# Performance work log

Hardware: AMD Instinct MI355X
Metric: run time of the kernel (lower is better)

## Reference

```python
import jax, jax.numpy as jnp
import numpy as np

B, T, C, H = 1, 4096, 3072, 24
D = C // H  # 128


def _make_rope_freqs(t, d):
    # comfy-style rotation matrices: [t, d//2, 2, 2] with rows [[cos,-sin],[sin,cos]]
    half = d // 2
    inv = 1.0 / (10000.0 ** (np.arange(half, dtype=np.float64) / half))
    ang = np.arange(t, dtype=np.float64)[:, None] * inv[None, :]
    cos, sin = np.cos(ang), np.sin(ang)
    f = np.stack([np.stack([cos, -sin], -1), np.stack([sin, cos], -1)], -2)
    return jnp.asarray(f, jnp.float32)


def setup_inputs() -> dict:
    key = jax.random.key(0)
    ks = jax.random.split(key, 6)
    s = 0.02  # typical init scale
    x = jax.random.normal(ks[0], (B, T, C), jnp.float32)
    context = jax.random.normal(ks[1], (B, T, C), jnp.float32)
    Wq = jax.random.normal(ks[2], (C, C), jnp.float32) * s
    Wk = jax.random.normal(ks[3], (C, C), jnp.float32) * s
    Wv = jax.random.normal(ks[4], (C, C), jnp.float32) * s
    Wo = jax.random.normal(ks[5], (C, C), jnp.float32) * s
    freqs = _make_rope_freqs(T, D)  # [T, D//2, 2, 2]
    return {"x": x, "context": context, "freqs": freqs,
            "Wq": Wq, "Wk": Wk, "Wv": Wv, "Wo": Wo}


def _apply_rope(t, freqs):
    # t: [B, T, H, D]; freqs: [T, D//2, 2, 2]
    b, tt, h, d = t.shape
    tr = t.reshape(b, tt, h, d // 2, 1, 2)
    f = freqs[:, None]  # [T, 1, D//2, 2, 2] -> broadcast over B, H
    out = f[..., 0] * tr[..., 0] + f[..., 1] * tr[..., 1]  # [B,T,H,D//2,2]
    return out.reshape(b, tt, h, d)


def reference(x, context, freqs, Wq, Wk, Wv, Wo):
    # QKV projections (torch Linear: y = x @ W.T), kept in BTHD layout
    q = (x @ Wq.T).reshape(B, T, H, D)
    k = (context @ Wk.T).reshape(B, -1, H, D)
    v = (context @ Wv.T).reshape(B, -1, H, D)
    # RoPE on q and k
    q = _apply_rope(q, freqs)
    k = _apply_rope(k, freqs)
    # SDPA, non-causal, scale 1/sqrt(D) (jax expects BTNH layout)
    out = jax.nn.dot_product_attention(q, k, v)
    return out.reshape(B, T, C) @ Wo.T
```

## Files before the change

### kernel.cpp

```cpp
#include <hip/hip_runtime.h>
#include <hip/hip_bf16.h>

#define TT 4096
#define CC 3072
#define HH 24
#define DD 128

typedef __bf16 bf16;
typedef __attribute__((ext_vector_type(8))) __bf16 bf16x8;
typedef __attribute__((ext_vector_type(4))) __bf16 bf16x4;
typedef __attribute__((ext_vector_type(4))) float f32x4;
typedef __attribute__((ext_vector_type(16))) float f32x16;
typedef __attribute__((ext_vector_type(4))) unsigned uint32x4;

#define MFMA(a,b,c)   __builtin_amdgcn_mfma_f32_16x16x32_bf16((a),(b),(c),0,0,0)
#define MFMA32(a,b,c) __builtin_amdgcn_mfma_f32_32x32x16_bf16((a),(b),(c),0,0,0)

static __device__ __forceinline__ unsigned cvtpk(float lo, float hi) {
  unsigned r;
  asm("v_cvt_pk_bf16_f32 %0, %1, %2" : "=v"(r) : "v"(lo), "v"(hi));
  return r;
}
static __device__ __forceinline__ float max3f(float a, float b, float c) {
  float r;
  asm("v_max3_f32 %0, %1, %2, %3" : "=v"(r) : "v"(a), "v"(b), "v"(c));
  return r;
}
static __device__ __forceinline__ void plswap(unsigned &x, unsigned &y) {
  asm volatile("v_permlane32_swap_b32 %0, %1" : "+v"(x), "+v"(y));
}

template<int ABF, int OBF>
__global__ __launch_bounds__(256, 2)
void gemm_nt(const void* __restrict__ Ap, const float* __restrict__ Bp,
             void* __restrict__ Cp, int M, int N, int K) {
  __shared__ bf16 As[2][128][40];
  __shared__ bf16 Bs[2][128][40];
  const int tid = threadIdx.x;
  const int lane = tid & 63, wid = tid >> 6;
  const int m0 = blockIdx.y * 128, n0 = blockIdx.x * 128;
  const int wr = (wid >> 1) * 64, wc = (wid & 1) * 64;
  const int r = lane & 15, g = lane >> 4;
  const float* Af = (const float*)Ap;
  const bf16*  Ab = (const bf16*)Ap;

  f32x4 acc[4][4] = {};
  f32x4 pa[4], pb[4];
  bf16x8 qa[2];

  const int NT = K >> 5;

  auto load_tiles = [&](int kt) {
    const int kk = kt * 32;
    if constexpr (ABF) {
      #pragma unroll
      for (int j = 0; j < 2; ++j) {
        int c = tid + 256*j, row = c >> 2, kc = c & 3;
        qa[j] = *(const bf16x8*)(Ab + (size_t)(m0+row)*K + kk + kc*8);
      }
    } else {
      #pragma unroll
      for (int j = 0; j < 4; ++j) {
        int c = tid + 256*j, row = c >> 3, kc = c & 7;
        pa[j] = *(const f32x4*)(Af + (size_t)(m0+row)*K + kk + kc*4);
      }
    }
    #pragma unroll
    for (int j = 0; j < 4; ++j) {
      int c = tid + 256*j, row = c >> 3, kc = c & 7;
      pb[j] = *(const f32x4*)(Bp + (size_t)(n0+row)*K + kk + kc*4);
    }
  };

  auto write_tiles = [&](int buf) {
    if constexpr (ABF) {
      #pragma unroll
      for (int j = 0; j < 2; ++j) {
        int c = tid + 256*j, row = c >> 2, kc = c & 3;
        *(bf16x8*)&As[buf][row][kc*8] = qa[j];
      }
    } else {
      #pragma unroll
      for (int j = 0; j < 4; ++j) {
        int c = tid + 256*j, row = c >> 3, kc = c & 7;
        bf16x4 b;
        b[0]=(bf16)pa[j][0]; b[1]=(bf16)pa[j][1]; b[2]=(bf16)pa[j][2]; b[3]=(bf16)pa[j][3];
        *(bf16x4*)&As[buf][row][kc*4] = b;
      }
    }
    #pragma unroll
    for (int j = 0; j < 4; ++j) {
      int c = tid + 256*j, row = c >> 3, kc = c & 7;
      bf16x4 b;
      b[0]=(bf16)pb[j][0]; b[1]=(bf16)pb[j][1]; b[2]=(bf16)pb[j][2]; b[3]=(bf16)pb[j][3];
      *(bf16x4*)&Bs[buf][row][kc*4] = b;
    }
  };

  load_tiles(0);
  write_tiles(0);
  __syncthreads();

  for (int kt = 0; kt < NT; ++kt) {
    const int cur = kt & 1;
    if (kt + 1 < NT) load_tiles(kt + 1);
    bf16x8 af[4], bfr[4];
    #pragma unroll
    for (int m = 0; m < 4; ++m) af[m]  = *(const bf16x8*)&As[cur][wr + m*16 + r][g*8];
    #pragma unroll
    for (int n = 0; n < 4; ++n) bfr[n] = *(const bf16x8*)&Bs[cur][wc + n*16 + r][g*8];
    #pragma unroll
    for (int m = 0; m < 4; ++m)
      #pragma unroll
      for (int n = 0; n < 4; ++n)
        acc[m][n] = MFMA(af[m], bfr[n], acc[m][n]);
    if (kt + 1 < NT) write_tiles((kt + 1) & 1);
    __syncthreads();
  }

  #pragma unroll
  for (int m = 0; m < 4; ++m)
    #pragma unroll
    for (int n = 0; n < 4; ++n) {
      const int col = n0 + wc + n*16 + r;
      #pragma unroll
      for (int j = 0; j < 4; ++j) {
        const int row = m0 + wr + m*16 + g*4 + j;
        float v = acc[m][n][j];
        if constexpr (OBF) ((bf16*)Cp)[(size_t)row*N + col] = (bf16)v;
        else               ((float*)Cp)[(size_t)row*N + col] = v;
      }
    }
}

__global__ __launch_bounds__(256)
void rope_kernel(bf16* __restrict__ X, const float* __restrict__ F, float scale) {
  const int i = blockIdx.x * 256 + threadIdx.x;
  const size_t e8 = (size_t)i * 8;
  const int t  = (int)(e8 / CC);
  const int c  = (int)(e8 % CC);
  const int hc = c & (DD - 1);
  const float4* f = (const float4*)(F + (size_t)t*256 + (hc>>1)*4);
  bf16x8 v = *(const bf16x8*)(X + e8);
  bf16x8 o;
  #pragma unroll
  for (int p = 0; p < 4; ++p) {
    float x0 = (float)v[2*p], x1 = (float)v[2*p+1];
    float4 ff = f[p];
    o[2*p]   = (bf16)((ff.x*x0 + ff.y*x1) * scale);
    o[2*p+1] = (bf16)((ff.z*x0 + ff.w*x1) * scale);
  }
  *(bf16x8*)(X + e8) = o;
}

__global__ __launch_bounds__(256)
void transpose_v(const bf16* __restrict__ V, bf16* __restrict__ Vt) {
  __shared__ bf16 tile[64 * 128];
  const int t0 = blockIdx.x * 64, h = blockIdx.y;
  const int tid = threadIdx.x;
  #pragma unroll
  for (int j = 0; j < 4; ++j) {
    int c = tid + 256*j, t = c >> 4, c16 = c & 15;
    uint4 val = *(const uint4*)(V + (size_t)(t0+t)*CC + h*DD + c16*8);
    int sw = ((t & 7) ^ ((t >> 3) & 7)) << 4;
    *(uint4*)((char*)tile + t*256 + ((c16*16) ^ sw)) = val;
  }
  __syncthreads();
  #pragma unroll
  for (int j = 0; j < 4; ++j) {
    int c = tid + 256*j, d = c >> 3, c8 = c & 7;
    bf16x8 o;
    #pragma unroll
    for (int i = 0; i < 8; ++i) {
      int t = c8*8 + i;
      int sw = ((t & 7) ^ ((t >> 3) & 7)) << 4;
      o[i] = *(const bf16*)((char*)tile + t*256 + ((d*2) ^ sw));
    }
    *(bf16x8*)(Vt + (size_t)(h*DD + d)*TT + t0 + c8*8) = o;
  }
}

__global__ __launch_bounds__(256, 3)
void attn_kernel(const bf16* __restrict__ Q, const bf16* __restrict__ Kb,
                 const bf16* __restrict__ Vt, bf16* __restrict__ O) {
  __shared__ bf16 Ks[64 * 128];
  __shared__ bf16 Vs[128 * 64];

  const int tid = threadIdx.x, lane = tid & 63, wid = tid >> 6;
  const int c31 = lane & 31, g2 = lane >> 5;

  const int bid = blockIdx.x;
  const int fid = (bid & 7) * 96 + (bid >> 3);
  const int h = fid >> 5, qt = fid & 31;
  const int qrow = qt * 128 + wid * 32 + c31;

  bf16x8 aq[8];
  {
    const bf16* qp = Q + (size_t)qrow * CC + h * DD + g2 * 8;
    #pragma unroll
    for (int d0 = 0; d0 < 8; ++d0) aq[d0] = *(const bf16x8*)(qp + d0 * 16);
  }

  float m_ = -1e30f, l_ = 0.f;
  f32x16 o_[4] = {};

  auto stage = [&](int kv0) {
    uint4 kr[4], vr4[4];
    #pragma unroll
    for (int j = 0; j < 4; ++j) {
      int cc = tid + 256*j, row = cc >> 4, c16 = cc & 15;
      kr[j] = *(const uint4*)(Kb + (size_t)(kv0 + row) * CC + h * DD + c16 * 8);
    }
    #pragma unroll
    for (int j = 0; j < 4; ++j) {
      int cc = tid + 256*j, row = cc >> 3, c8 = cc & 7;
      vr4[j] = *(const uint4*)(Vt + (size_t)(h * DD + row) * TT + kv0 + c8 * 8);
    }
    #pragma unroll
    for (int j = 0; j < 4; ++j) {
      int cc = tid + 256*j, row = cc >> 4, c16 = cc & 15;
      *(uint4*)((char*)Ks + row * 256 + ((c16 * 16) ^ ((row & 15) << 4))) = kr[j];
    }
    #pragma unroll
    for (int j = 0; j < 4; ++j) {
      int cc = tid + 256*j, row = cc >> 3, c8 = cc & 7;
      *(uint4*)((char*)Vs + row * 128 + ((c8 * 16) ^ ((row & 7) << 4))) = vr4[j];
    }
  };

  const int NT = TT / 64;
  for (int t = 0; t < NT; ++t) {
    if (t) __syncthreads();
    stage(t * 64);
    __syncthreads();

    f32x16 s[2] = {};
    __builtin_amdgcn_s_setprio(1);
    #pragma unroll
    for (int d0 = 0; d0 < 8; ++d0) {
      #pragma unroll
      for (int tt = 0; tt < 2; ++tt) {
        const int kvr = tt * 32 + c31;
        bf16x8 ak = *(const bf16x8*)((const char*)Ks + kvr * 256 +
                                     ((d0 * 32 + g2 * 16) ^ ((kvr & 15) << 4)));
        s[tt] = MFMA32(ak, aq[d0], s[tt]);
      }
    }
    __builtin_amdgcn_s_setprio(0);

    float mx = fmaxf(s[0][0], s[0][1]);
    #pragma unroll
    for (int i = 2; i < 16; i += 2) mx = max3f(mx, s[0][i], s[0][i+1]);
    #pragma unroll
    for (int i = 0; i < 16; i += 2) mx = max3f(mx, s[1][i], s[1][i+1]);
    mx = fmaxf(mx, __shfl_xor(mx, 32, 64));
    if (!__all(mx <= m_ + 8.f)) {
      float mn = fmaxf(m_, mx);
      float al = __builtin_amdgcn_exp2f(m_ - mn);
      l_ *= al;
      #pragma unroll
      for (int d0 = 0; d0 < 4; ++d0) o_[d0] *= al;
      m_ = mn;
    }

    unsigned w0[8], w1[8];
    float rs = 0.f;
    #pragma unroll
    for (int jj = 0; jj < 8; ++jj) {
      float a0 = __builtin_amdgcn_exp2f(s[0][2*jj] - m_);
      float b0 = __builtin_amdgcn_exp2f(s[0][2*jj+1] - m_);
      float a1 = __builtin_amdgcn_exp2f(s[1][2*jj] - m_);
      float b1 = __builtin_amdgcn_exp2f(s[1][2*jj+1] - m_);
      rs += (a0 + b0) + (a1 + b1);
      w0[jj] = cvtpk(a0, b0);
      w1[jj] = cvtpk(a1, b1);
    }
    rs += __shfl_xor(rs, 32, 64);
    l_ += rs;

    bf16x8 pb[4];
    #pragma unroll
    for (int t2 = 0; t2 < 4; ++t2) {
      const int jA = (t2 & 1) * 4;
      unsigned x0, y0, x1, y1;
      if (t2 < 2) { x0 = w0[jA]; y0 = w0[jA+2]; x1 = w0[jA+1]; y1 = w0[jA+3]; }
      else        { x0 = w1[jA]; y0 = w1[jA+2]; x1 = w1[jA+1]; y1 = w1[jA+3]; }
      plswap(x0, y0);
      plswap(x1, y1);
      uint32x4 uu; uu[0] = x0; uu[1] = x1; uu[2] = y0; uu[3] = y1;
      pb[t2] = __builtin_bit_cast(bf16x8, uu);
    }

    __builtin_amdgcn_s_setprio(1);
    #pragma unroll
    for (int d0 = 0; d0 < 4; ++d0) {
      const int vr = d0 * 32 + c31;
      #pragma unroll
      for (int t2 = 0; t2 < 4; ++t2) {
        bf16x8 av = *(const bf16x8*)((const char*)Vs + vr * 128 +
                                     ((t2 * 32 + g2 * 16) ^ ((vr & 7) << 4)));
        o_[d0] = MFMA32(av, pb[t2], o_[d0]);
      }
    }
    __builtin_amdgcn_s_setprio(0);
  }

  const float inv = 1.f / l_;
  bf16* orow = O + (size_t)qrow * CC + h * DD;
  #pragma unroll
  for (int d0 = 0; d0 < 4; ++d0)
    #pragma unroll
    for (int q4 = 0; q4 < 4; ++q4) {
      uint2 val;
      val.x = cvtpk(o_[d0][q4*4 + 0] * inv, o_[d0][q4*4 + 1] * inv);
      val.y = cvtpk(o_[d0][q4*4 + 2] * inv, o_[d0][q4*4 + 3] * inv);
      *(uint2*)(orow + d0*32 + q4*8 + g2*4) = val;
    }
}

extern "C" void kernel_launch(void* const* d_in, const int* in_sizes, int n_in,
                              void* d_out, int out_size, void* d_ws, size_t ws_size,
                              hipStream_t stream) {
  const float* x   = (const float*)d_in[0];
  const float* ctx = (const float*)d_in[1];
  const float* fr  = (const float*)d_in[2];
  const float* Wq  = (const float*)d_in[3];
  const float* Wk  = (const float*)d_in[4];
  const float* Wv  = (const float*)d_in[5];
  const float* Wo  = (const float*)d_in[6];
  float* out = (float*)d_out;
  char* ws = (char*)d_ws;

  const size_t SZ = (size_t)TT * CC * sizeof(bf16);
  bf16* Qb  = (bf16*)(ws);
  bf16* Kbf = (bf16*)(ws + SZ);
  bf16* Vb  = (bf16*)(ws + 2*SZ);
  bf16* Vtb = (bf16*)(ws + 3*SZ);
  bf16* Ob  = Vb;

  dim3 gg(CC/128, TT/128);
  gemm_nt<0,1><<<gg, 256, 0, stream>>>(x,   Wq, Qb,  TT, CC, CC);
  gemm_nt<0,1><<<gg, 256, 0, stream>>>(ctx, Wk, Kbf, TT, CC, CC);
  gemm_nt<0,1><<<gg, 256, 0, stream>>>(ctx, Wv, Vb,  TT, CC, CC);

  const int rblocks = (TT*CC/8)/256;
  rope_kernel<<<rblocks, 256, 0, stream>>>(Qb,  fr, 0.12751743314942355f);
  rope_kernel<<<rblocks, 256, 0, stream>>>(Kbf, fr, 1.0f);

  transpose_v<<<dim3(TT/64, HH), 256, 0, stream>>>(Vb, Vtb);
  attn_kernel<<<dim3(768), 256, 0, stream>>>(Qb, Kbf, Vtb, Ob);

  gemm_nt<1,0><<<gg, 256, 0, stream>>>(Ob, Wo, out, TT, CC, CC);
}
```

Baseline: 827.3 us.

## Pre-convert inputs to bf16, use direct-to-LDS GEMM loads, prefetch attention KV

Adds a bf16 conversion pass for x, context and all four weight matrices, then runs a new GEMM that streams bf16 tiles straight into LDS with global_load_lds instead of loading fp32 through registers and converting in-loop. The attention kernel now issues the next KV tile's global loads before computing on the current one, overlapping memory latency with MFMA work. The bf16 path is used only when the workspace is large enough and falls back to the old path otherwise. The new GEMM is single-buffered with two barriers per k-step, and the conversion kernels add extra memory traffic.

```diff
diff --git a/kernel.cpp b/kernel.cpp
--- a/kernel.cpp
+++ b/kernel.cpp
@@ -28,6 +28,78 @@
 }
 static __device__ __forceinline__ void plswap(unsigned &x, unsigned &y) {
   asm volatile("v_permlane32_swap_b32 %0, %1" : "+v"(x), "+v"(y));
+}
+static __device__ __forceinline__ void gl16(const bf16* g, bf16* l) {
+  __builtin_amdgcn_global_load_lds(
+      (const __attribute__((address_space(1))) unsigned int*)(g),
+      (__attribute__((address_space(3))) unsigned int*)(l), 16, 0, 0);
+}
+
+__global__ __launch_bounds__(256)
+void cvt_bf16(const float* __restrict__ in, bf16* __restrict__ out, int n8) {
+  int i = blockIdx.x * 256 + threadIdx.x;
+  const int stride = gridDim.x * 256;
+  for (; i < n8; i += stride) {
+    const float4* p = (const float4*)(in + (size_t)i * 8);
+    float4 a = p[0], b = p[1];
+    bf16x8 o;
+    o[0]=(bf16)a.x; o[1]=(bf16)a.y; o[2]=(bf16)a.z; o[3]=(bf16)a.w;
+    o[4]=(bf16)b.x; o[5]=(bf16)b.y; o[6]=(bf16)b.z; o[7]=(bf16)b.w;
+    *(bf16x8*)(out + (size_t)i * 8) = o;
+  }
+}
+
+template<int OBF>
+__global__ __launch_bounds__(256, 2)
+void gemm_bt(const bf16* __restrict__ A, const bf16* __restrict__ B,
+             void* __restrict__ Cp, int M, int N, int K) {
+  __shared__ bf16 As[128 * 32];
+  __shared__ bf16 Bs[128 * 32];
+  const int tid = threadIdx.x, lane = tid & 63, wid = tid >> 6;
+  const int m0 = blockIdx.y * 128, n0 = blockIdx.x * 128;
+  const int wr = (wid >> 1) * 64, wc = (wid & 1) * 64;
+  const int r = lane & 15, g = lane >> 4;
+  const int srow = lane >> 2, scol = (lane & 3) * 8;
+
+  f32x4 acc[4][4] = {};
+  const int NT = K >> 5;
+
+  for (int kt = 0; kt < NT; ++kt) {
+    const int kk = kt << 5;
+    if (kt) __syncthreads();
+    #pragma unroll
+    for (int j = 0; j < 2; ++j) {
+      const int base = (wid * 2 + j) * 16;
+      gl16(A + (size_t)(m0 + base + srow) * K + kk + scol, As + base * 32);
+      gl16(B + (size_t)(n0 + base + srow) * K + kk + scol, Bs + base * 32);
+    }
+    __syncthreads();
+
+    bf16x8 af[4], bfr[4];
+    #pragma unroll
+    for (int m = 0; m < 4; ++m) af[m]  = *(const bf16x8*)&As[(wr + m*16 + r)*32 + g*8];
+    #pragma unroll
+    for (int n = 0; n < 4; ++n) bfr[n] = *(const bf16x8*)&Bs[(wc + n*16 + r)*32 + g*8];
+    #pragma unroll
+    for (int m = 0; m < 4; ++m)
+      #pragma unroll
+      for (int n = 0; n < 4; ++n)
+        acc[m][n] = MFMA(af[m], bfr[n], acc[m][n]);
+  }
+
+  #pragma unroll
+  for (int m = 0; m < 4; ++m)
+    #pragma unroll
+    for (int n = 0; n < 4; ++n) {
+      const int col = n0 + wc + n*16 + r;
+      #pragma unroll
+      for (int j = 0; j < 4; ++j) {
+        const int row = m0 + wr + m*16 + g*4 + j;
+        float v = acc[m][n][j];
+        if constexpr (OBF) ((bf16*)Cp)[(size_t)row*N + col] = (bf16)v;
+        else               ((float*)Cp)[(size_t)row*N + col] = v;
+      }
+    }
 }
 
 template<int ABF, int OBF>
@@ -47,7 +119,6 @@
   f32x4 acc[4][4] = {};
   f32x4 pa[4], pb[4];
   bf16x8 qa[2];
-
   const int NT = K >> 5;
 
   auto load_tiles = [&](int kt) {
@@ -71,7 +142,6 @@
       pb[j] = *(const f32x4*)(Bp + (size_t)(n0+row)*K + kk + kc*4);
     }
   };
-
   auto write_tiles = [&](int buf) {
     if constexpr (ABF) {
       #pragma unroll
@@ -100,7 +170,6 @@
   load_tiles(0);
   write_tiles(0);
   __syncthreads();
-
   for (int kt = 0; kt < NT; ++kt) {
     const int cur = kt & 1;
     if (kt + 1 < NT) load_tiles(kt + 1);
@@ -117,7 +186,6 @@
     if (kt + 1 < NT) write_tiles((kt + 1) & 1);
     __syncthreads();
   }
-
   #pragma unroll
   for (int m = 0; m < 4; ++m)
     #pragma unroll
@@ -204,8 +272,8 @@
   float m_ = -1e30f, l_ = 0.f;
   f32x16 o_[4] = {};
 
-  auto stage = [&](int kv0) {
-    uint4 kr[4], vr4[4];
+  uint4 kr[4], vr4[4];
+  auto issue = [&](int kv0) {
     #pragma unroll
     for (int j = 0; j < 4; ++j) {
       int cc = tid + 256*j, row = cc >> 4, c16 = cc & 15;
@@ -216,6 +284,8 @@
       int cc = tid + 256*j, row = cc >> 3, c8 = cc & 7;
       vr4[j] = *(const uint4*)(Vt + (size_t)(h * DD + row) * TT + kv0 + c8 * 8);
     }
+  };
+  auto write_lds = [&]() {
     #pragma unroll
     for (int j = 0; j < 4; ++j) {
       int cc = tid + 256*j, row = cc >> 4, c16 = cc & 15;
@@ -227,12 +297,15 @@
       *(uint4*)((char*)Vs + row * 128 + ((c8 * 16) ^ ((row & 7) << 4))) = vr4[j];
     }
   };
+
+  issue(0);
 
   const int NT = TT / 64;
   for (int t = 0; t < NT; ++t) {
     if (t) __syncthreads();
-    stage(t * 64);
+    write_lds();
     __syncthreads();
+    if (t + 1 < NT) issue((t + 1) * 64);
 
     f32x16 s[2] = {};
     __builtin_amdgcn_s_setprio(1);
@@ -331,24 +404,54 @@
   float* out = (float*)d_out;
   char* ws = (char*)d_ws;
 
-  const size_t SZ = (size_t)TT * CC * sizeof(bf16);
+  const size_t SZ  = (size_t)TT * CC * sizeof(bf16);
+  const size_t WSZ = (size_t)CC * CC * sizeof(bf16);
   bf16* Qb  = (bf16*)(ws);
   bf16* Kbf = (bf16*)(ws + SZ);
   bf16* Vb  = (bf16*)(ws + 2*SZ);
   bf16* Vtb = (bf16*)(ws + 3*SZ);
   bf16* Ob  = Vb;
 
-  dim3 gg(CC/128, TT/128);
-  gemm_nt<0,1><<<gg, 256, 0, stream>>>(x,   Wq, Qb,  TT, CC, CC);
-  gemm_nt<0,1><<<gg, 256, 0, stream>>>(ctx, Wk, Kbf, TT, CC, CC);
-  gemm_nt<0,1><<<gg, 256, 0, stream>>>(ctx, Wv, Vb,  TT, CC, CC);
-
   const int rblocks = (TT*CC/8)/256;
-  rope_kernel<<<rblocks, 256, 0, stream>>>(Qb,  fr, 0.12751743314942355f);
-  rope_kernel<<<rblocks, 256, 0, stream>>>(Kbf, fr, 1.0f);
-
-  transpose_v<<<dim3(TT/64, HH), 256, 0, stream>>>(Vb, Vtb);
-  attn_kernel<<<dim3(768), 256, 0, stream>>>(Qb, Kbf, Vtb, Ob);
-
-  gemm_nt<1,0><<<gg, 256, 0, stream>>>(Ob, Wo, out, TT, CC, CC);
-}
+  const float QSCALE = 0.12751743314942355f;
+
+  const size_t NEED = 5*SZ + 3*WSZ;
+  if (ws_size >= NEED) {
+    bf16* xb   = Vtb;
+    bf16* ctxb = (bf16*)(ws + 4*SZ);
+    bf16* Wqb  = (bf16*)(ws + 5*SZ);
+    bf16* Wkb  = (bf16*)(ws + 5*SZ + WSZ);
+    bf16* Wvb  = (bf16*)(ws + 5*SZ + 2*WSZ);
+    bf16* Wob  = Wqb;
+
+    cvt_bf16<<<2048, 256, 0, stream>>>(x,   xb,   TT*CC/8);
+    cvt_bf16<<<2048, 256, 0, stream>>>(ctx, ctxb, TT*CC/8);
+    cvt_bf16<<<2048, 256, 0, stream>>>(Wq,  Wqb,  CC*CC/8);
+    cvt_bf16<<<2048, 256, 0, stream>>>(Wk,  Wkb,  CC*CC/8);
+    cvt_bf16<<<2048, 256, 0, stream>>>(Wv,  Wvb,  CC*CC/8);
+
+    dim3 gg(CC/128, TT/128);
+    gemm_bt<1><<<gg, 256, 0, stream>>>(xb,   Wqb, Qb,  TT, CC, CC);
+    gemm_bt<1><<<gg, 256, 0, stream>>>(ctxb, Wkb, Kbf, TT, CC, CC);
+    gemm_bt<1><<<gg, 256, 0, stream>>>(ctxb, Wvb, Vb,  TT, CC, CC);
+
+    rope_kernel<<<rblocks, 256, 0, stream>>>(Qb,  fr, QSCALE);
+    rope_kernel<<<rblocks, 256, 0, stream>>>(Kbf, fr, 1.0f);
+
+    transpose_v<<<dim3(TT/64, HH), 256, 0, stream>>>(Vb, Vtb);
+    cvt_bf16<<<2048, 256, 0, stream>>>(Wo, Wob, CC*CC/8);
+    attn_kernel<<<dim3(768), 256, 0, stream>>>(Qb, Kbf, Vtb, Ob);
+
+    gemm_bt<0><<<gg, 256, 0, stream>>>(Ob, Wob, out, TT, CC, CC);
+  } else {
+    dim3 gg(CC/128, TT/128);
+    gemm_nt<0,1><<<gg, 256, 0, stream>>>(x,   Wq, Qb,  TT, CC, CC);
+    gemm_nt<0,1><<<gg, 256, 0, stream>>>(ctx, Wk, Kbf, TT, CC, CC);
+    gemm_nt<0,1><<<gg, 256, 0, stream>>>(ctx, Wv, Vb,  TT, CC, CC);
+    rope_kernel<<<rblocks, 256, 0, stream>>>(Qb,  fr, QSCALE);
+    rope_kernel<<<rblocks, 256, 0, stream>>>(Kbf, fr, 1.0f);
+    transpose_v<<<dim3(TT/64, HH), 256, 0, stream>>>(Vb, Vtb);
+    attn_kernel<<<dim3(768), 256, 0, stream>>>(Qb, Kbf, Vtb, Ob);
+    gemm_nt<1,0><<<gg, 256, 0, stream>>>(Ob, Wo, out, TT, CC, CC);
+  }
+}
```

Result: slower. 1.026 ms (+24.0%).
